# Optimization experiments

Hardware: AMD Instinct MI355X
Metric: run time of the kernel (lower is better)

## Reference

```python
import jax, jax.numpy as jnp
import numpy as np

VOC, D, CPR, RELS = 2048, 128, 128, 7
B, DEPTH = 512, 4  # complete binary trees: 2**DEPTH leaves per tree


def setup_inputs() -> dict:
    key = jax.random.key(0)
    ks = jax.random.split(key, 13)
    s = lambda k, shape, fan: jax.random.normal(k, shape, jnp.float32) / np.sqrt(fan)
    return {
        "leaf_ids": jax.random.randint(ks[0], (B, 2, 2 ** DEPTH), 0, VOC),
        "Wv": s(ks[1], (D, VOC), VOC), "bv": jnp.zeros((D,), jnp.float32),
        "Wcps": s(ks[2], (D, 2 * D), 2 * D), "bcps": jnp.zeros((D,), jnp.float32),
        "Wcpst": s(ks[3], (D, D * D), D * D), "bcpst": jnp.zeros((D,), jnp.float32),
        "Wcpr": s(ks[4], (CPR, 2 * D), 2 * D), "bcpr": jnp.zeros((CPR,), jnp.float32),
        "Wcprt": s(ks[5], (CPR, D * D), D * D), "bcprt": jnp.zeros((CPR,), jnp.float32),
        "Wsm": s(ks[6], (RELS, CPR), CPR), "bsm": jnp.zeros((RELS,), jnp.float32),
    }


def reference(leaf_ids, Wv, bv, Wcps, bcps, Wcpst, bcpst, Wcpr, bcpr, Wcprt, bcprt, Wsm, bsm):
    d = Wv.shape[0]
    # leaf embedding: voc(one_hot(idx)) == Wv[:, idx] + bv  -> [B, 2, L, d]
    h = jnp.take(Wv.T, leaf_ids, axis=0) + bv
    # batched level-by-level tree composition (complete binary trees)
    while h.shape[2] > 1:
        l, r = h[:, :, 0::2, :], h[:, :, 1::2, :]
        lin = jnp.concatenate([l, r], axis=-1) @ Wcps.T + bcps
        kron = (l[..., :, None] * r[..., None, :]).reshape(l.shape[:-1] + (d * d,))
        h = jnp.tanh(lin + kron @ Wcpst.T + bcpst)
    lc, rc = h[:, 0, 0, :], h[:, 1, 0, :]  # [B, d] each
    cpr = jnp.concatenate([lc, rc], axis=-1) @ Wcpr.T + bcpr
    kron = (lc[:, :, None] * rc[:, None, :]).reshape(lc.shape[0], d * d)
    act = jax.nn.leaky_relu(cpr + kron @ Wcprt.T + bcprt, 0.01)
    logits = act @ Wsm.T + bsm
    return jax.nn.log_softmax(logits, axis=-1)  # [B, RELS]
```

## Files before the change

### kernel.cpp

```cpp
#include <hip/hip_runtime.h>
#include <hip/hip_bf16.h>
#include <hip/hip_fp16.h>

#define DD    128
#define VOCAB 2048
#define NRELS 7
#define NWF   (130 * 16384)

typedef _Float16 f16;
typedef __attribute__((ext_vector_type(8))) _Float16 f16x8;
typedef __attribute__((ext_vector_type(4))) float    f32x4;

__device__ __forceinline__ float lde(const void* p, size_t i, int bf) {
    if (bf) return (float)((const __hip_bfloat16*)p)[i];
    return ((const float*)p)[i];
}

__global__ void detect_kernel(const unsigned short* __restrict__ wv, int* __restrict__ flag)
{
    if (threadIdx.x == 0 && blockIdx.x == 0) {
        int sane = 0;
        for (int i = 0; i < 64; ++i) {
            unsigned e = (wv[i] >> 7) & 0xFFu;
            if (e >= 90u && e <= 160u) ++sane;
        }
        *flag = (sane == 64) ? 1 : 0;
    }
}

__global__ void prep_kernel(const void* Wv, const void* bv, const void* Wcps, const void* bcps,
                            const void* Wcpst, const void* bcpst, const void* Wcpr, const void* bcpr,
                            const void* Wcprt, const void* bcprt, const void* Wsm, const void* bsm,
                            const int* __restrict__ flag,
                            f16* __restrict__ WvT, f16* __restrict__ Wext, f16* __restrict__ Wfin,
                            float* __restrict__ bias_lvl, float* __restrict__ bias_fin,
                            float* __restrict__ Wsm_f, float* __restrict__ bsm_f)
{
    const int bf = *flag;
    long idx = (long)blockIdx.x * 256 + threadIdx.x;
    const long nWvT = (long)VOCAB * DD;
    if (idx < nWvT) {
        int v = (int)(idx >> 7), d = (int)(idx & 127);
        WvT[idx] = (f16)(lde(Wv, (size_t)d * VOCAB + v, bf) + lde(bv, d, bf));
        return;
    }
    idx -= nWvT;
    if (idx < 2 * (long)NWF) {
        f16* dst = (idx < NWF) ? Wext : Wfin;
        const void* Wt = (idx < NWF) ? Wcpst : Wcprt;
        const void* Ws = (idx < NWF) ? Wcps  : Wcpr;
        long id2 = (idx < NWF) ? idx : idx - NWF;
        int i   = (int)(id2 >> 14);
        int rem = (int)(id2 & 16383);
        int n8  = rem >> 11;
        int t   = (rem >> 9) & 3;
        int ln  = (rem >> 3) & 63;
        int e   = rem & 7;
        int nn   = n8 * 16 + (ln & 15);
        int koff = t * 32 + ((ln >> 4) << 3) + e;
        float val = (i < 128) ? lde(Wt, (size_t)nn * 16384 + (size_t)i * 128 + koff, bf)
                              : lde(Ws, (size_t)nn * 256 + (size_t)(i - 128) * 128 + koff, bf);
        dst[id2] = (f16)val;
        return;
    }
    idx -= 2 * (long)NWF;
    if (idx < 128)            bias_lvl[idx] = lde(bcps, idx, bf) + lde(bcpst, idx, bf);
    else if (idx < 256)       bias_fin[idx - 128] = lde(bcpr, idx - 128, bf) + lde(bcprt, idx - 128, bf);
    else if (idx < 256 + 896) Wsm_f[idx - 256] = lde(Wsm, idx - 256, bf);
    else if (idx < 256 + 896 + NRELS) bsm_f[idx - 256 - 896] = lde(bsm, idx - 256 - 896, bf);
}

__global__ void embed_kernel(const int* __restrict__ ids,
                             const f16* __restrict__ WvT, f16* __restrict__ h0)
{
    int t = blockIdx.x * 256 + threadIdx.x;
    int row = t >> 4;
    int c = (t & 15) * 8;
    int id = ids[row];
    *(f16x8*)&h0[(size_t)row * DD + c] = *(const f16x8*)&WvT[(size_t)id * DD + c];
}

__launch_bounds__(128, 2)
__global__ void gemm_kernel(const f16* __restrict__ hin, const f16* __restrict__ Wf,
                            f16* __restrict__ part, int Mrows, int S, int BI)
{
    __shared__ f16 Lt[64 * 128];

    const int tid  = threadIdx.x;
    const int lane = tid & 63;
    const int wv   = tid >> 6;
    const int s    = blockIdx.x % S;
    const int mb   = blockIdx.x / S;
    const int m0   = mb * 64;
    const int i0   = s * BI;
    const int nI   = BI + ((s == 0) ? 2 : 0);
    const int NSt  = nI * 4;

    #pragma unroll
    for (int it = 0; it < 8; ++it) {
        int c  = it * 128 + tid;
        int mm = c >> 4;
        int cb = c & 15;
        f16x8 v = *(const f16x8*)&hin[(size_t)(2 * (m0 + mm)) * DD + cb * 8];
        *(f16x8*)&Lt[mm * 128 + ((cb ^ (mm & 15)) << 3)] = v;
    }

    const int mrow = lane & 15;
    const int q    = lane >> 4;

    f16x8 rf[4][4];
    #pragma unroll
    for (int mt = 0; mt < 4; ++mt)
        #pragma unroll
        for (int t = 0; t < 4; ++t)
            rf[mt][t] = *(const f16x8*)&hin[(size_t)(2 * (m0 + mt * 16 + mrow) + 1) * DD + t * 32 + q * 8];

    __syncthreads();

    auto imap = [&](int ii) { return (ii < BI) ? (i0 + ii) : (128 + ii - BI); };
    const f16* wb0 = Wf + wv * 8192 + lane * 8;
    auto ldW = [&](int st, f16x8* d) {
        int i = imap(st >> 2), t = st & 3;
        const f16* p = wb0 + (size_t)i * 16384 + t * 512;
        #pragma unroll
        for (int nt = 0; nt < 4; ++nt) d[nt] = *(const f16x8*)(p + nt * 2048);
    };
    auto lpRead = [&](int i, int mt) -> f16 {
        return Lt[(mt * 16 + mrow) * 128 + (((i >> 3) ^ mrow) << 3) + (i & 7)];
    };

    f32x4 acc[4][4] = {};
    f16x8 wbuf[2][4];
    f16 lpv[4], lpn[4];

    ldW(0, wbuf[0]);
    {
        int i = imap(0);
        if (i < 128) {
            #pragma unroll
            for (int mt = 0; mt < 4; ++mt) lpv[mt] = lpRead(i, mt);
        }
    }

    for (int ii = 0; ii < nI; ++ii) {
        const int i = imap(ii);
        f16x8 lb[4];
        if (i < 128) {
            #pragma unroll
            for (int mt = 0; mt < 4; ++mt) {
                f16 v = lpv[mt];
                #pragma unroll
                for (int e = 0; e < 8; ++e) lb[mt][e] = v;
            }
        }
        #pragma unroll
        for (int t = 0; t < 4; ++t) {
            const int st = ii * 4 + t;
            if (st + 1 < NSt) ldW(st + 1, wbuf[(t + 1) & 1]);
            if (t == 1 && ii + 1 < nI) {
                int i2 = imap(ii + 1);
                if (i2 < 128) {
                    #pragma unroll
                    for (int mt = 0; mt < 4; ++mt) lpn[mt] = lpRead(i2, mt);
                }
            }
            const f16x8* wc = wbuf[t & 1];
            if (i < 128) {
                #pragma unroll
                for (int mt = 0; mt < 4; ++mt) {
                    f16x8 a = lb[mt] * rf[mt][t];
                    #pragma unroll
                    for (int nt = 0; nt < 4; ++nt)
                        acc[mt][nt] = __builtin_amdgcn_mfma_f32_16x16x32_f16(a, wc[nt], acc[mt][nt], 0, 0, 0);
                }
            } else if (i == 128) {
                #pragma unroll
                for (int mt = 0; mt < 4; ++mt) {
                    f16x8 a = *(const f16x8*)&Lt[(mt * 16 + mrow) * 128 + (((t * 4 + q) ^ mrow) << 3)];
                    #pragma unroll
                    for (int nt = 0; nt < 4; ++nt)
                        acc[mt][nt] = __builtin_amdgcn_mfma_f32_16x16x32_f16(a, wc[nt], acc[mt][nt], 0, 0, 0);
                }
            } else {
                #pragma unroll
                for (int mt = 0; mt < 4; ++mt) {
                    #pragma unroll
                    for (int nt = 0; nt < 4; ++nt)
                        acc[mt][nt] = __builtin_amdgcn_mfma_f32_16x16x32_f16(rf[mt][t], wc[nt], acc[mt][nt], 0, 0, 0);
                }
            }
        }
        #pragma unroll
        for (int mt = 0; mt < 4; ++mt) lpv[mt] = lpn[mt];
    }

    f16* pb = part + ((size_t)s * Mrows + m0) * DD;
    #pragma unroll
    for (int mt = 0; mt < 4; ++mt)
        #pragma unroll
        for (int nt = 0; nt < 4; ++nt) {
            int colg = wv * 64 + nt * 16 + mrow;
            #pragma unroll
            for (int r = 0; r < 4; ++r) {
                int rowl = mt * 16 + q * 4 + r;
                pb[(size_t)rowl * DD + colg] = (f16)acc[mt][nt][r];
            }
        }
}

__global__ void epi_level(const f16* __restrict__ part, const float* __restrict__ bias,
                          f16* __restrict__ hout, int Mrows, int S)
{
    int idx = (blockIdx.x * 256 + threadIdx.x) * 8;
    size_t stride = (size_t)Mrows * DD;
    float sum[8] = {};
    for (int s2 = 0; s2 < S; ++s2) {
        f16x8 v = *(const f16x8*)&part[(size_t)s2 * stride + idx];
        #pragma unroll
        for (int e = 0; e < 8; ++e) sum[e] += (float)v[e];
    }
    int n = idx & 127;
    f16x8 o;
    #pragma unroll
    for (int e = 0; e < 8; ++e) o[e] = (f16)tanhf(sum[e] + bias[n + e]);
    *(f16x8*)&hout[idx] = o;
}

__global__ void fin_epi(const f16* __restrict__ part, const float* __restrict__ bias,
                        const float* __restrict__ Wsm_f, const float* __restrict__ bsm_f,
                        const int* __restrict__ flag, void* __restrict__ outp, int S)
{
    int lane = threadIdx.x & 63;
    int wv = threadIdx.x >> 6;
    int p = blockIdx.x * 4 + wv;
    size_t stride = (size_t)512 * DD;
    const f16* base = part + (size_t)p * DD;
    float a0 = 0.f, a1 = 0.f;
    for (int s2 = 0; s2 < S; ++s2) {
        a0 += (float)base[(size_t)s2 * stride + lane];
        a1 += (float)base[(size_t)s2 * stride + 64 + lane];
    }
    a0 += bias[lane];      a1 += bias[64 + lane];
    a0 = (a0 > 0.f) ? a0 : 0.01f * a0;
    a1 = (a1 > 0.f) ? a1 : 0.01f * a1;
    float lg[NRELS];
    #pragma unroll
    for (int r = 0; r < NRELS; ++r) {
        float pr = a0 * Wsm_f[r * DD + lane] + a1 * Wsm_f[r * DD + 64 + lane];
        #pragma unroll
        for (int d = 1; d < 64; d <<= 1) pr += __shfl_xor(pr, d, 64);
        lg[r] = pr + bsm_f[r];
    }
    float mx = lg[0];
    #pragma unroll
    for (int r = 1; r < NRELS; ++r) mx = fmaxf(mx, lg[r]);
    float se = 0.f;
    #pragma unroll
    for (int r = 0; r < NRELS; ++r) se += expf(lg[r] - mx);
    float lse = logf(se) + mx;
    if (lane < NRELS) {
        float v = lg[lane] - lse;
        if (*flag) ((__hip_bfloat16*)outp)[p * NRELS + lane] = __float2bfloat16(v);
        else       ((float*)outp)[p * NRELS + lane] = v;
    }
}

extern "C" void kernel_launch(void* const* d_in, const int* in_sizes, int n_in,
                              void* d_out, int out_size, void* d_ws, size_t ws_size,
                              hipStream_t stream)
{
    const int* ids = (const int*)d_in[0];

    char* ws = (char*)d_ws;
    f16*   part     = (f16*)ws;
    f16*   h0       = (f16*)(ws + ((size_t)16 << 20));
    f16*   h1       = (f16*)(ws + ((size_t)20 << 20));
    f16*   h2       = (f16*)(ws + ((size_t)22 << 20));
    f16*   h3       = (f16*)(ws + ((size_t)23 << 20));
    f16*   h4       = (f16*)(ws + ((size_t)23 << 20) + (512 << 10));
    f16*   WvT      = (f16*)(ws + ((size_t)24 << 20));
    f16*   Wext     = (f16*)(ws + ((size_t)24 << 20) + (512 << 10));
    f16*   Wfin     = Wext + (size_t)NWF;
    float* bias_lvl = (float*)(Wfin + (size_t)NWF);
    float* bias_fin = bias_lvl + 128;
    int*   flag     = (int*)(bias_fin + 128);
    float* Wsm_f    = (float*)(flag + 16);
    float* bsm_f    = Wsm_f + NRELS * DD;

    if (ws_size < ((size_t)34 << 20)) return;

    detect_kernel<<<1, 64, 0, stream>>>((const unsigned short*)d_in[1], flag);
    prep_kernel<<<17669, 256, 0, stream>>>(d_in[1], d_in[2], d_in[3], d_in[4], d_in[5], d_in[6],
                                           d_in[7], d_in[8], d_in[9], d_in[10], d_in[11], d_in[12],
                                           flag, WvT, Wext, Wfin, bias_lvl, bias_fin, Wsm_f, bsm_f);
    embed_kernel<<<1024, 256, 0, stream>>>(ids, WvT, h0);

    gemm_kernel<<<1024, 128, 0, stream>>>(h0, Wext, part, 8192, 8, 16);
    epi_level<<<512, 256, 0, stream>>>(part, bias_lvl, h1, 8192, 8);
    gemm_kernel<<<1024, 128, 0, stream>>>(h1, Wext, part, 4096, 16, 8);
    epi_level<<<256, 256, 0, stream>>>(part, bias_lvl, h2, 4096, 16);
    gemm_kernel<<<1024, 128, 0, stream>>>(h2, Wext, part, 2048, 32, 4);
    epi_level<<<128, 256, 0, stream>>>(part, bias_lvl, h3, 2048, 32);
    gemm_kernel<<<1024, 128, 0, stream>>>(h3, Wext, part, 1024, 64, 2);
    epi_level<<<64, 256, 0, stream>>>(part, bias_lvl, h4, 1024, 64);
    gemm_kernel<<<1024, 128, 0, stream>>>(h4, Wfin, part, 512, 128, 1);
    fin_epi<<<128, 256, 0, stream>>>(part, bias_fin, Wsm_f, bsm_f, flag, d_out, 128);
}
```

Baseline: 309.0 us.

## Tile weight prep through shared memory and retile GEMM into 128-row blocks

The monolithic prep kernel is split into two kernels. One transposes Wv through a shared-memory tile, and the other gathers each 16-row weight chunk into shared memory so the MFMA-layout output is written with coalesced stores instead of strided per-element global reads. The GEMM blocks now cover 128 rows with each wavefront owning 64 rows and the block owning a 64-column half, so each weight load is reused across more rows. The two linear-term weight slices are split across split-K indices 1 and 2 to balance work. This doubles shared memory per block and changes the block-to-tile mapping, which affects occupancy and load balance.

```diff
diff --git a/kernel.cpp b/kernel.cpp
--- a/kernel.cpp
+++ b/kernel.cpp
@@ -28,46 +28,65 @@
     }
 }
 
-__global__ void prep_kernel(const void* Wv, const void* bv, const void* Wcps, const void* bcps,
-                            const void* Wcpst, const void* bcpst, const void* Wcpr, const void* bcpr,
-                            const void* Wcprt, const void* bcprt, const void* Wsm, const void* bsm,
-                            const int* __restrict__ flag,
-                            f16* __restrict__ WvT, f16* __restrict__ Wext, f16* __restrict__ Wfin,
-                            float* __restrict__ bias_lvl, float* __restrict__ bias_fin,
-                            float* __restrict__ Wsm_f, float* __restrict__ bsm_f)
+__global__ void prep_wvt(const void* Wv, const void* bv, const int* __restrict__ flag,
+                         f16* __restrict__ WvT)
 {
     const int bf = *flag;
-    long idx = (long)blockIdx.x * 256 + threadIdx.x;
-    const long nWvT = (long)VOCAB * DD;
-    if (idx < nWvT) {
-        int v = (int)(idx >> 7), d = (int)(idx & 127);
-        WvT[idx] = (f16)(lde(Wv, (size_t)d * VOCAB + v, bf) + lde(bv, d, bf));
+    __shared__ float tile[64][65];
+    int vt = blockIdx.x >> 1;
+    int dt = blockIdx.x & 1;
+    int tx = threadIdx.x & 63, ty = threadIdx.x >> 6;
+    for (int yy = ty; yy < 64; yy += 4)
+        tile[yy][tx] = lde(Wv, (size_t)(dt * 64 + yy) * VOCAB + vt * 64 + tx, bf);
+    __syncthreads();
+    for (int yy = ty; yy < 64; yy += 4) {
+        int v = vt * 64 + yy, d = dt * 64 + tx;
+        WvT[(size_t)v * DD + d] = (f16)(tile[tx][yy] + lde(bv, d, bf));
+    }
+}
+
+__global__ void prep_wf(const void* Wcps, const void* Wcpst, const void* Wcpr, const void* Wcprt,
+                        const void* bcps, const void* bcpst, const void* bcpr, const void* bcprt,
+                        const void* Wsm, const void* bsm, const int* __restrict__ flag,
+                        f16* __restrict__ Wext, f16* __restrict__ Wfin,
+                        float* __restrict__ bias_lvl, float* __restrict__ bias_fin,
+                        float* __restrict__ Wsm_f, float* __restrict__ bsm_f)
+{
+    const int bf = *flag;
+    const int b = blockIdx.x;
+    const int tid = threadIdx.x;
+    if (b >= 2080) {
+        if (tid < 128)      bias_lvl[tid] = lde(bcps, tid, bf) + lde(bcpst, tid, bf);
+        else if (tid < 256) bias_fin[tid - 128] = lde(bcpr, tid - 128, bf) + lde(bcprt, tid - 128, bf);
+        for (int o = tid; o < NRELS * DD; o += 256) Wsm_f[o] = lde(Wsm, o, bf);
+        if (tid < NRELS) bsm_f[tid] = lde(bsm, tid, bf);
         return;
     }
-    idx -= nWvT;
-    if (idx < 2 * (long)NWF) {
-        f16* dst = (idx < NWF) ? Wext : Wfin;
-        const void* Wt = (idx < NWF) ? Wcpst : Wcprt;
-        const void* Ws = (idx < NWF) ? Wcps  : Wcpr;
-        long id2 = (idx < NWF) ? idx : idx - NWF;
-        int i   = (int)(id2 >> 14);
-        int rem = (int)(id2 & 16383);
-        int n8  = rem >> 11;
-        int t   = (rem >> 9) & 3;
-        int ln  = (rem >> 3) & 63;
-        int e   = rem & 7;
-        int nn   = n8 * 16 + (ln & 15);
-        int koff = t * 32 + ((ln >> 4) << 3) + e;
-        float val = (i < 128) ? lde(Wt, (size_t)nn * 16384 + (size_t)i * 128 + koff, bf)
-                              : lde(Ws, (size_t)nn * 256 + (size_t)(i - 128) * 128 + koff, bf);
-        dst[id2] = (f16)val;
-        return;
-    }
-    idx -= 2 * (long)NWF;
-    if (idx < 128)            bias_lvl[idx] = lde(bcps, idx, bf) + lde(bcpst, idx, bf);
-    else if (idx < 256)       bias_fin[idx - 128] = lde(bcpr, idx - 128, bf) + lde(bcprt, idx - 128, bf);
-    else if (idx < 256 + 896) Wsm_f[idx - 256] = lde(Wsm, idx - 256, bf);
-    else if (idx < 256 + 896 + NRELS) bsm_f[idx - 256 - 896] = lde(bsm, idx - 256 - 896, bf);
+    const int which = b / 1040;
+    const int rem   = b - which * 1040;
+    const int i     = rem >> 3;
+    const int n8    = rem & 7;
+    const void* Wt = which ? (const void*)Wcprt : (const void*)Wcpst;
+    const void* Ws = which ? (const void*)Wcpr  : (const void*)Wcps;
+    f16* dst = which ? Wfin : Wext;
+
+    __shared__ float tile[16 * 129];
+    #pragma unroll
+    for (int it = 0; it < 8; ++it) {
+        int idx = it * 256 + tid;
+        int rr = idx >> 7, c = idx & 127;
+        float v = (i < 128) ? lde(Wt, (size_t)(n8 * 16 + rr) * 16384 + (size_t)i * 128 + c, bf)
+                            : lde(Ws, (size_t)(n8 * 16 + rr) * 256 + (size_t)(i - 128) * 128 + c, bf);
+        tile[rr * 129 + c] = v;
+    }
+    __syncthreads();
+    f16* out = dst + (size_t)(i * 8 + n8) * 2048;
+    #pragma unroll
+    for (int it = 0; it < 8; ++it) {
+        int o = it * 256 + tid;
+        int t = o >> 9, ln = (o >> 3) & 63, e = o & 7;
+        out[o] = (f16)tile[(ln & 15) * 129 + t * 32 + ((ln >> 4) << 3) + e];
+    }
 }
 
 __global__ void embed_kernel(const int* __restrict__ ids,
@@ -84,20 +103,23 @@
 __global__ void gemm_kernel(const f16* __restrict__ hin, const f16* __restrict__ Wf,
                             f16* __restrict__ part, int Mrows, int S, int BI)
 {
-    __shared__ f16 Lt[64 * 128];
+    __shared__ f16 Lt[128 * 128];
 
     const int tid  = threadIdx.x;
     const int lane = tid & 63;
     const int wv   = tid >> 6;
-    const int s    = blockIdx.x % S;
-    const int mb   = blockIdx.x / S;
-    const int m0   = mb * 64;
+    const int b    = blockIdx.x;
+    const int nh   = (b >> 2) & 1;
+    const int r    = ((b >> 3) << 2) | (b & 3);
+    const int mb   = r / S;
+    const int s    = r - mb * S;
+    const int m0   = mb * 128;
     const int i0   = s * BI;
-    const int nI   = BI + ((s == 0) ? 2 : 0);
+    const int nI   = BI + ((s == 1 || s == 2) ? 1 : 0);
     const int NSt  = nI * 4;
 
     #pragma unroll
-    for (int it = 0; it < 8; ++it) {
+    for (int it = 0; it < 16; ++it) {
         int c  = it * 128 + tid;
         int mm = c >> 4;
         int cb = c & 15;
@@ -107,18 +129,19 @@
 
     const int mrow = lane & 15;
     const int q    = lane >> 4;
+    const int wm   = wv * 64;
 
     f16x8 rf[4][4];
     #pragma unroll
     for (int mt = 0; mt < 4; ++mt)
         #pragma unroll
         for (int t = 0; t < 4; ++t)
-            rf[mt][t] = *(const f16x8*)&hin[(size_t)(2 * (m0 + mt * 16 + mrow) + 1) * DD + t * 32 + q * 8];
+            rf[mt][t] = *(const f16x8*)&hin[(size_t)(2 * (m0 + wm + mt * 16 + mrow) + 1) * DD + t * 32 + q * 8];
 
     __syncthreads();
 
-    auto imap = [&](int ii) { return (ii < BI) ? (i0 + ii) : (128 + ii - BI); };
-    const f16* wb0 = Wf + wv * 8192 + lane * 8;
+    auto imap = [&](int ii) { return (ii < BI) ? (i0 + ii) : (s == 1 ? 128 : 129); };
+    const f16* wb0 = Wf + nh * 8192 + lane * 8;
     auto ldW = [&](int st, f16x8* d) {
         int i = imap(st >> 2), t = st & 3;
         const f16* p = wb0 + (size_t)i * 16384 + t * 512;
@@ -126,7 +149,7 @@
         for (int nt = 0; nt < 4; ++nt) d[nt] = *(const f16x8*)(p + nt * 2048);
     };
     auto lpRead = [&](int i, int mt) -> f16 {
-        return Lt[(mt * 16 + mrow) * 128 + (((i >> 3) ^ mrow) << 3) + (i & 7)];
+        return Lt[(wm + mt * 16 + mrow) * 128 + (((i >> 3) ^ mrow) << 3) + (i & 7)];
     };
 
     f32x4 acc[4][4] = {};
@@ -176,7 +199,7 @@
             } else if (i == 128) {
                 #pragma unroll
                 for (int mt = 0; mt < 4; ++mt) {
-                    f16x8 a = *(const f16x8*)&Lt[(mt * 16 + mrow) * 128 + (((t * 4 + q) ^ mrow) << 3)];
+                    f16x8 a = *(const f16x8*)&Lt[(wm + mt * 16 + mrow) * 128 + (((t * 4 + q) ^ mrow) << 3)];
                     #pragma unroll
                     for (int nt = 0; nt < 4; ++nt)
                         acc[mt][nt] = __builtin_amdgcn_mfma_f32_16x16x32_f16(a, wc[nt], acc[mt][nt], 0, 0, 0);
@@ -194,16 +217,16 @@
         for (int mt = 0; mt < 4; ++mt) lpv[mt] = lpn[mt];
     }
 
-    f16* pb = part + ((size_t)s * Mrows + m0) * DD;
+    f16* pb = part + ((size_t)s * Mrows + m0) * DD + nh * 64;
     #pragma unroll
     for (int mt = 0; mt < 4; ++mt)
         #pragma unroll
         for (int nt = 0; nt < 4; ++nt) {
-            int colg = wv * 64 + nt * 16 + mrow;
+            int colg = nt * 16 + mrow;
             #pragma unroll
-            for (int r = 0; r < 4; ++r) {
-                int rowl = mt * 16 + q * 4 + r;
-                pb[(size_t)rowl * DD + colg] = (f16)acc[mt][nt][r];
+            for (int rr = 0; rr < 4; ++rr) {
+                int rowl = wm + mt * 16 + q * 4 + rr;
+                pb[(size_t)rowl * DD + colg] = (f16)acc[mt][nt][rr];
             }
         }
 }
@@ -290,9 +313,11 @@
     if (ws_size < ((size_t)34 << 20)) return;
 
     detect_kernel<<<1, 64, 0, stream>>>((const unsigned short*)d_in[1], flag);
-    prep_kernel<<<17669, 256, 0, stream>>>(d_in[1], d_in[2], d_in[3], d_in[4], d_in[5], d_in[6],
-                                           d_in[7], d_in[8], d_in[9], d_in[10], d_in[11], d_in[12],
-                                           flag, WvT, Wext, Wfin, bias_lvl, bias_fin, Wsm_f, bsm_f);
+    prep_wvt<<<64, 256, 0, stream>>>(d_in[1], d_in[2], flag, WvT);
+    prep_wf<<<2081, 256, 0, stream>>>(d_in[3], d_in[5], d_in[7], d_in[9],
+                                      d_in[4], d_in[6], d_in[8], d_in[10],
+                                      d_in[11], d_in[12], flag,
+                                      Wext, Wfin, bias_lvl, bias_fin, Wsm_f, bsm_f);
     embed_kernel<<<1024, 256, 0, stream>>>(ids, WvT, h0);
 
     gemm_kernel<<<1024, 128, 0, stream>>>(h0, Wext, part, 8192, 8, 16);
```

Result: no change. 311.0 us (+0.6%).
